# Optimization experiments

Hardware: AMD Instinct MI355X
Metric: run time of the kernel (lower is better)

Reference implementation:

```python
import jax, jax.numpy as jnp
import numpy as np

# EKV constants from Config
VT = 0.025
N_FACTOR = 1.5
VD = 0.5
ALPHA = 2e-06
BASE_TIA = 500000.0

KERNEL = 3
STRIDE = 1
PAD = 1


def _unfold(x, k, stride, pad):
    # torch.nn.functional.unfold: (N, C, H, W) -> (N, C*k*k, L), patch dims ordered (c, kh, kw)
    N, C, H, W = x.shape
    xp = jnp.pad(x, ((0, 0), (0, 0), (pad, pad), (pad, pad)))
    Ho = (H + 2 * pad - k) // stride + 1
    Wo = (W + 2 * pad - k) // stride + 1
    patches = []
    for i in range(k):
        for j in range(k):
            patches.append(xp[:, :, i:i + stride * Ho:stride, j:j + stride * Wo:stride])
    # (k*k, N, C, Ho, Wo) -> (N, C, k*k, Ho*Wo) -> (N, C*k*k, L)
    p = jnp.stack(patches, axis=2)  # (N, C, k*k, Ho, Wo)
    return p.reshape(N, C * k * k, Ho * Wo), Ho, Wo


def setup_inputs() -> dict:
    key = jax.random.key(0)
    k1, k2 = jax.random.split(key)
    x = jax.random.normal(k1, (4, 64, 32, 32), dtype=jnp.float32)
    # theta ~ Normal(2.5, 0.5), shape (out_channels, in_channels, k, k)
    theta = 2.5 + 0.5 * jax.random.normal(k2, (64, 64, 3, 3), dtype=jnp.float32)
    return {"x": x, "theta": theta}


def reference(x, theta):
    N, C, H, W = x.shape
    O = theta.shape[0]
    fan_in = C * KERNEL * KERNEL
    tia_gain = BASE_TIA / (fan_in ** 0.5)
    phi = 2 * N_FACTOR * VT

    x_unf, Ho, Wo = _unfold(x, KERNEL, STRIDE, PAD)      # (N, C*k*k, L)
    x_in = x_unf[:, None, :, :]                           # (N, 1, CKK, L)
    w_th = theta.reshape(1, O, -1, 1)                     # (1, O, CKK, 1)

    v_diff = x_in - w_th                                  # (N, O, CKK, L)
    f_term = jnp.square(jax.nn.softplus(v_diff / phi))
    r_term = jnp.square(jax.nn.softplus((v_diff - VD) / phi))
    i_syn = ALPHA * (f_term - r_term)
    out_current = jnp.sum(i_syn, axis=2)                  # (N, O, L)
    out_voltage = out_current * tia_gain
    return out_voltage.reshape(N, O, Ho, Wo)
```

## Files before the change

### kernel.cpp

```cpp
#include <hip/hip_runtime.h>
#include <math.h>

#define HH 32
#define WW 32
#define CIN 64
#define NO 64
#define NCK 576
#define X_ELEMS 262144
#define STRIDE_E 296

#define WS_W    0
#define WS_TAU  36864

__device__ __forceinline__ float fexp2(float x) {
#if __has_builtin(__builtin_amdgcn_exp2f)
    return __builtin_amdgcn_exp2f(x);
#else
    return exp2f(x);
#endif
}
__device__ __forceinline__ float flog2(float x) {
#if __has_builtin(__builtin_amdgcn_logf)
    return __builtin_amdgcn_logf(x);
#else
    return log2f(x);
#endif
}

__global__ __launch_bounds__(256) void prep_kernel(const float* __restrict__ theta,
                                                   float* __restrict__ ws) {
    constexpr float SZ = 19.235933878519512f;
    const int b = blockIdx.x, t = threadIdx.x;
    if (b < 144) {
        int i = b * 256 + t;
        int o = i & 63, ck = i >> 6;
        float th = theta[o * NCK + ck];
        ws[WS_W + i] = -SZ * th;
        float mn = th;
#pragma unroll
        for (int s = 32; s > 0; s >>= 1)
            mn = fminf(mn, __shfl_xor(mn, s, 64));
        if (o == 0) ws[WS_TAU + ck] = SZ * mn - 8.0f;
    } else {
        if (t < 64) ws[WS_TAU + NCK + t] = 1e30f;
    }
}

__global__ __launch_bounds__(512) void ekv_kernel(
        const float* __restrict__ x, const float* __restrict__ ws,
        float* __restrict__ out) {
    constexpr float SZ = 19.235933878519512f;
    constexpr float C2 = 1.2726342e-3f;
    constexpr float OS = 0.020018875579925058f;

    __shared__ int   lc[8][STRIDE_E];
    __shared__ float lx[8][STRIDE_E];
    __shared__ float pp[8][64];

    const int t    = threadIdx.x;
    const int lane = t & 63;
    const int wv   = __builtin_amdgcn_readfirstlane(t >> 6);
    const int p2   = (int)blockIdx.x * 8 + wv;
    const int pix  = p2 >> 1, half = p2 & 1;
    const int n  = pix >> 10;
    const int ho = (pix >> 5) & 31;
    const int wo = pix & 31;
    const int c0 = half * 32;

    int l = lane;
    int c_off = l / 9; if (c_off > 6) c_off = 6;
    int k = l - 9 * c_off; if (k > 8) k = 8;
    int di = k / 3, dj = k - 3 * (k / 3);
    int h = ho + di - 1, w_ = wo + dj - 1;
    bool sval = (h >= 0) && (h < HH) && (w_ >= 0) && (w_ < WW);
    int hc = min(max(h, 0), HH - 1), wc = min(max(w_, 0), WW - 1);
    float msc = ((l < 63) && sval) ? SZ : 0.0f;

    int gidx = n * (CIN * HH * WW) + (c0 + c_off) * 1024 + hc * WW + wc;
    const float* tw = ws + WS_TAU + c0 * 9;

    int cnt = 0;
    float xv = x[min(gidx, X_ELEMS - 1)];
    float tv = tw[l];

    for (int cb = 0; cb < 32; cb += 7) {
        int cc = 32 - cb; if (cc > 7) cc = 7;
        int gidx2 = gidx + 7 * 1024;
        const float* tw2 = tw + 63;
        float xvn = xv, tvn = tv;
        if (cb + 7 < 32) { xvn = x[min(gidx2, X_ELEMS - 1)]; tvn = tw2[l]; }

        float xs = xv * msc;
        bool a = (xs >= tv) && (l < cc * 9);
        unsigned long long act = __ballot(a);
        unsigned lo32 = (unsigned)act, hi32 = (unsigned)(act >> 32);
        int idx = __builtin_amdgcn_mbcnt_hi(hi32,
                      __builtin_amdgcn_mbcnt_lo(lo32, 0));
        if (a) {
            lc[wv][cnt + idx] = (c0 + cb) * 9 + l;
            lx[wv][cnt + idx] = xs;
        }
        cnt += (int)__popcll(act);
        gidx = gidx2; tw = tw2; xv = xvn; tv = tvn;
    }
    int padn = (-cnt) & 7;
    if (lane < padn) { lc[wv][cnt + lane] = 0; lx[wv][cnt + lane] = -100000.0f; }
    const int rounds = (cnt + padn) >> 3;

    const int4*   LC = (const int4*)&lc[wv][0];
    const float4* LX = (const float4*)&lx[wv][0];
    const float* wsW = ws + WS_W + lane;

    float accF0 = 0.f, accR0 = 0.f, accF1 = 0.f, accR1 = 0.f;

#define EKV_BODY(SX, WV, AF, AR)                                           \
    {                                                                      \
        float z  = (WV) + (SX);                        \
        float e  = fexp2(z);                                               \
        float f  = flog2(1.0f + e);                                        \
        float rr = flog2(fmaf(C2, e, 1.0f));                               \
        AF = fmaf(f, f, AF);                                               \
        AR = fmaf(rr, rr, AR);                                             \
    }

    if (rounds > 0) {
        int4   ca = LC[0], cb4 = LC[1];
        float4 xa = LX[0], xb = LX[1];
        for (int r = 0; r < rounds; ++r) {
            int4 can = ca, cbn = cb4; float4 xan = xa, xbn = xb;
            if (r + 1 < rounds) {
                can = LC[2 * r + 2]; cbn = LC[2 * r + 3];
                xan = LX[2 * r + 2]; xbn = LX[2 * r + 3];
            }
            float W0 = wsW[ca.x  << 6];
            float W1 = wsW[ca.y  << 6];
            float W2 = wsW[ca.z  << 6];
            float W3 = wsW[ca.w  << 6];
            float W4 = wsW[cb4.x << 6];
            float W5 = wsW[cb4.y << 6];
            float W6 = wsW[cb4.z << 6];
            float W7 = wsW[cb4.w << 6];
            EKV_BODY(xa.x, W0, accF0, accR0)
            EKV_BODY(xa.y, W1, accF1, accR1)
            EKV_BODY(xa.z, W2, accF0, accR0)
            EKV_BODY(xa.w, W3, accF1, accR1)
            EKV_BODY(xb.x, W4, accF0, accR0)
            EKV_BODY(xb.y, W5, accF1, accR1)
            EKV_BODY(xb.z, W6, accF0, accR0)
            EKV_BODY(xb.w, W7, accF1, accR1)
            ca = can; cb4 = cbn; xa = xan; xb = xbn;
        }
    }
#undef EKV_BODY

    pp[wv][lane] = (accF0 + accF1) - (accR0 + accR1);
    __syncthreads();
    if (t < 64) {
        float s0 = (pp[0][t] + pp[1][t]) * OS;
        float s1 = (pp[2][t] + pp[3][t]) * OS;
        float s2 = (pp[4][t] + pp[5][t]) * OS;
        float s3 = (pp[6][t] + pp[7][t]) * OS;
        int pixb = (int)blockIdx.x * 4;
        int nn = pixb >> 10, hh = (pixb >> 5) & 31, w0 = pixb & 31;
        float4 v = make_float4(s0, s1, s2, s3);
        *(float4*)&out[((nn * NO + t) * HH + hh) * WW + w0] = v;
    }
}

extern "C" void kernel_launch(void* const* d_in, const int* in_sizes, int n_in,
                              void* d_out, int out_size, void* d_ws, size_t ws_size,
                              hipStream_t stream) {
    const float* x     = (const float*)d_in[0];
    const float* theta = (const float*)d_in[1];
    float* out = (float*)d_out;
    float* ws  = (float*)d_ws;

    prep_kernel<<<145, 256, 0, stream>>>(theta, ws);
    ekv_kernel <<<1024, 512, 0, stream>>>(x, ws, out);
}
```

Measured before the change: 73.21 us.

## Fuse prep and EKV kernels into one cooperative launch with grid sync

Merges the theta-preprocessing kernel and the main EKV kernel into a single cooperative kernel. The first 73 blocks write the scaled weights and thresholds, then a grid-wide sync makes them visible before compute. The grid is halved to 512 blocks, and each block now handles two pixel units of 8 waves and writes two float4 outputs. This removes one kernel launch and the gap between the two kernels. In exchange it adds a grid barrier, needs all 512 blocks to be co-resident, and gives each block more serial work.

```diff
diff --git a/kernel.cpp b/kernel.cpp
--- a/kernel.cpp
+++ b/kernel.cpp
@@ -1,5 +1,8 @@
 #include <hip/hip_runtime.h>
+#include <hip/hip_cooperative_groups.h>
 #include <math.h>
+
+namespace cg = cooperative_groups;
 
 #define HH 32
 #define WW 32
@@ -27,12 +30,24 @@
 #endif
 }
 
-__global__ __launch_bounds__(256) void prep_kernel(const float* __restrict__ theta,
-                                                   float* __restrict__ ws) {
+__global__ __launch_bounds__(512, 4) void ekv_fused(
+        const float* __restrict__ x, const float* __restrict__ theta,
+        float* __restrict__ ws, float* __restrict__ out) {
     constexpr float SZ = 19.235933878519512f;
-    const int b = blockIdx.x, t = threadIdx.x;
-    if (b < 144) {
-        int i = b * 256 + t;
+    constexpr float C2 = 1.2726342e-3f;
+    constexpr float OS = 0.020018875579925058f;
+
+    __shared__ int   lc[8][STRIDE_E];
+    __shared__ float lx[8][STRIDE_E];
+    __shared__ float pp[16][64];
+
+    const int t    = threadIdx.x;
+    const int lane = t & 63;
+    const int wv   = __builtin_amdgcn_readfirstlane(t >> 6);
+    const int bb   = (int)blockIdx.x;
+
+    if (bb < 72) {
+        int i = bb * 512 + t;
         int o = i & 63, ck = i >> 6;
         float th = theta[o * NCK + ck];
         ws[WS_W + i] = -SZ * th;
@@ -41,129 +56,124 @@
         for (int s = 32; s > 0; s >>= 1)
             mn = fminf(mn, __shfl_xor(mn, s, 64));
         if (o == 0) ws[WS_TAU + ck] = SZ * mn - 8.0f;
-    } else {
+    } else if (bb == 72) {
         if (t < 64) ws[WS_TAU + NCK + t] = 1e30f;
     }
-}
+    __threadfence();
+    cg::this_grid().sync();
 
-__global__ __launch_bounds__(512) void ekv_kernel(
-        const float* __restrict__ x, const float* __restrict__ ws,
-        float* __restrict__ out) {
-    constexpr float SZ = 19.235933878519512f;
-    constexpr float C2 = 1.2726342e-3f;
-    constexpr float OS = 0.020018875579925058f;
+    for (int unit = 0; unit < 2; ++unit) {
+        const int p2  = bb * 16 + wv + unit * 8;
+        const int pix = p2 >> 1, half = p2 & 1;
+        const int n  = pix >> 10;
+        const int ho = (pix >> 5) & 31;
+        const int wo = pix & 31;
+        const int c0 = half * 32;
 
-    __shared__ int   lc[8][STRIDE_E];
-    __shared__ float lx[8][STRIDE_E];
-    __shared__ float pp[8][64];
+        int l = lane;
+        int c_off = l / 9; if (c_off > 6) c_off = 6;
+        int k = l - 9 * c_off; if (k > 8) k = 8;
+        int di = k / 3, dj = k - 3 * (k / 3);
+        int h = ho + di - 1, w_ = wo + dj - 1;
+        bool sval = (h >= 0) && (h < HH) && (w_ >= 0) && (w_ < WW);
+        int hc = min(max(h, 0), HH - 1), wc = min(max(w_, 0), WW - 1);
+        float msc = ((l < 63) && sval) ? SZ : 0.0f;
 
-    const int t    = threadIdx.x;
-    const int lane = t & 63;
-    const int wv   = __builtin_amdgcn_readfirstlane(t >> 6);
-    const int p2   = (int)blockIdx.x * 8 + wv;
-    const int pix  = p2 >> 1, half = p2 & 1;
-    const int n  = pix >> 10;
-    const int ho = (pix >> 5) & 31;
-    const int wo = pix & 31;
-    const int c0 = half * 32;
+        int gidx = n * (CIN * HH * WW) + (c0 + c_off) * 1024 + hc * WW + wc;
+        const float* tw = ws + WS_TAU + c0 * 9;
 
-    int l = lane;
-    int c_off = l / 9; if (c_off > 6) c_off = 6;
-    int k = l - 9 * c_off; if (k > 8) k = 8;
-    int di = k / 3, dj = k - 3 * (k / 3);
-    int h = ho + di - 1, w_ = wo + dj - 1;
-    bool sval = (h >= 0) && (h < HH) && (w_ >= 0) && (w_ < WW);
-    int hc = min(max(h, 0), HH - 1), wc = min(max(w_, 0), WW - 1);
-    float msc = ((l < 63) && sval) ? SZ : 0.0f;
+        int cnt = 0;
+        float xv = x[min(gidx, X_ELEMS - 1)];
+        float tv = tw[l];
 
-    int gidx = n * (CIN * HH * WW) + (c0 + c_off) * 1024 + hc * WW + wc;
-    const float* tw = ws + WS_TAU + c0 * 9;
+        for (int cb = 0; cb < 32; cb += 7) {
+            int cc = 32 - cb; if (cc > 7) cc = 7;
+            int gidx2 = gidx + 7 * 1024;
+            const float* tw2 = tw + 63;
+            float xvn = xv, tvn = tv;
+            if (cb + 7 < 32) { xvn = x[min(gidx2, X_ELEMS - 1)]; tvn = tw2[l]; }
 
-    int cnt = 0;
-    float xv = x[min(gidx, X_ELEMS - 1)];
-    float tv = tw[l];
+            float xs = xv * msc;
+            bool a = (xs >= tv) && (l < cc * 9);
+            unsigned long long act = __ballot(a);
+            unsigned lo32 = (unsigned)act, hi32 = (unsigned)(act >> 32);
+            int idx = __builtin_amdgcn_mbcnt_hi(hi32,
+                          __builtin_amdgcn_mbcnt_lo(lo32, 0));
+            if (a) {
+                lc[wv][cnt + idx] = (c0 + cb) * 9 + l;
+                lx[wv][cnt + idx] = xs;
+            }
+            cnt += (int)__popcll(act);
+            gidx = gidx2; tw = tw2; xv = xvn; tv = tvn;
+        }
+        int padn = (-cnt) & 7;
+        if (lane < padn) { lc[wv][cnt + lane] = 0; lx[wv][cnt + lane] = -100000.0f; }
+        const int rounds = (cnt + padn) >> 3;
 
-    for (int cb = 0; cb < 32; cb += 7) {
-        int cc = 32 - cb; if (cc > 7) cc = 7;
-        int gidx2 = gidx + 7 * 1024;
-        const float* tw2 = tw + 63;
-        float xvn = xv, tvn = tv;
-        if (cb + 7 < 32) { xvn = x[min(gidx2, X_ELEMS - 1)]; tvn = tw2[l]; }
+        const int4*   LC = (const int4*)&lc[wv][0];
+        const float4* LX = (const float4*)&lx[wv][0];
+        const float* wsW = ws + WS_W + lane;
 
-        float xs = xv * msc;
-        bool a = (xs >= tv) && (l < cc * 9);
-        unsigned long long act = __ballot(a);
-        unsigned lo32 = (unsigned)act, hi32 = (unsigned)(act >> 32);
-        int idx = __builtin_amdgcn_mbcnt_hi(hi32,
-                      __builtin_amdgcn_mbcnt_lo(lo32, 0));
-        if (a) {
-            lc[wv][cnt + idx] = (c0 + cb) * 9 + l;
-            lx[wv][cnt + idx] = xs;
-        }
-        cnt += (int)__popcll(act);
-        gidx = gidx2; tw = tw2; xv = xvn; tv = tvn;
-    }
-    int padn = (-cnt) & 7;
-    if (lane < padn) { lc[wv][cnt + lane] = 0; lx[wv][cnt + lane] = -100000.0f; }
-    const int rounds = (cnt + padn) >> 3;
-
-    const int4*   LC = (const int4*)&lc[wv][0];
-    const float4* LX = (const float4*)&lx[wv][0];
-    const float* wsW = ws + WS_W + lane;
-
-    float accF0 = 0.f, accR0 = 0.f, accF1 = 0.f, accR1 = 0.f;
+        float accF0 = 0.f, accR0 = 0.f, accF1 = 0.f, accR1 = 0.f;
 
 #define EKV_BODY(SX, WV, AF, AR)                                           \
-    {                                                                      \
-        float z  = (WV) + (SX);                        \
-        float e  = fexp2(z);                                               \
-        float f  = flog2(1.0f + e);                                        \
-        float rr = flog2(fmaf(C2, e, 1.0f));                               \
-        AF = fmaf(f, f, AF);                                               \
-        AR = fmaf(rr, rr, AR);                                             \
+        {                                                                  \
+            float z  = (WV) + (SX);                    \
+            float e  = fexp2(z);                                           \
+            float f  = flog2(1.0f + e);                                    \
+            float rr = flog2(fmaf(C2, e, 1.0f));                           \
+            AF = fmaf(f, f, AF);                                           \
+            AR = fmaf(rr, rr, AR);                                         \
+        }
+
+        if (rounds > 0) {
+            int4   ca = LC[0], cb4 = LC[1];
+            float4 xa = LX[0], xb = LX[1];
+            for (int r = 0; r < rounds; ++r) {
+                int4 can = ca, cbn = cb4; float4 xan = xa, xbn = xb;
+                if (r + 1 < rounds) {
+                    can = LC[2 * r + 2]; cbn = LC[2 * r + 3];
+                    xan = LX[2 * r + 2]; xbn = LX[2 * r + 3];
+                }
+                float W0 = wsW[ca.x  << 6];
+                float W1 = wsW[ca.y  << 6];
+                float W2 = wsW[ca.z  << 6];
+                float W3 = wsW[ca.w  << 6];
+                float W4 = wsW[cb4.x << 6];
+                float W5 = wsW[cb4.y << 6];
+                float W6 = wsW[cb4.z << 6];
+                float W7 = wsW[cb4.w << 6];
+                EKV_BODY(xa.x, W0, accF0, accR0)
+                EKV_BODY(xa.y, W1, accF1, accR1)
+                EKV_BODY(xa.z, W2, accF0, accR0)
+                EKV_BODY(xa.w, W3, accF1, accR1)
+                EKV_BODY(xb.x, W4, accF0, accR0)
+                EKV_BODY(xb.y, W5, accF1, accR1)
+                EKV_BODY(xb.z, W6, accF0, accR0)
+                EKV_BODY(xb.w, W7, accF1, accR1)
+                ca = can; cb4 = cbn; xa = xan; xb = xbn;
+            }
+        }
+#undef EKV_BODY
+
+        pp[wv + unit * 8][lane] = (accF0 + accF1) - (accR0 + accR1);
     }
 
-    if (rounds > 0) {
-        int4   ca = LC[0], cb4 = LC[1];
-        float4 xa = LX[0], xb = LX[1];
-        for (int r = 0; r < rounds; ++r) {
-            int4 can = ca, cbn = cb4; float4 xan = xa, xbn = xb;
-            if (r + 1 < rounds) {
-                can = LC[2 * r + 2]; cbn = LC[2 * r + 3];
-                xan = LX[2 * r + 2]; xbn = LX[2 * r + 3];
-            }
-            float W0 = wsW[ca.x  << 6];
-            float W1 = wsW[ca.y  << 6];
-            float W2 = wsW[ca.z  << 6];
-            float W3 = wsW[ca.w  << 6];
-            float W4 = wsW[cb4.x << 6];
-            float W5 = wsW[cb4.y << 6];
-            float W6 = wsW[cb4.z << 6];
-            float W7 = wsW[cb4.w << 6];
-            EKV_BODY(xa.x, W0, accF0, accR0)
-            EKV_BODY(xa.y, W1, accF1, accR1)
-            EKV_BODY(xa.z, W2, accF0, accR0)
-            EKV_BODY(xa.w, W3, accF1, accR1)
-            EKV_BODY(xb.x, W4, accF0, accR0)
-            EKV_BODY(xb.y, W5, accF1, accR1)
-            EKV_BODY(xb.z, W6, accF0, accR0)
-            EKV_BODY(xb.w, W7, accF1, accR1)
-            ca = can; cb4 = cbn; xa = xan; xb = xbn;
-        }
-    }
-#undef EKV_BODY
-
-    pp[wv][lane] = (accF0 + accF1) - (accR0 + accR1);
     __syncthreads();
     if (t < 64) {
-        float s0 = (pp[0][t] + pp[1][t]) * OS;
-        float s1 = (pp[2][t] + pp[3][t]) * OS;
-        float s2 = (pp[4][t] + pp[5][t]) * OS;
-        float s3 = (pp[6][t] + pp[7][t]) * OS;
-        int pixb = (int)blockIdx.x * 4;
+        float s0 = (pp[ 0][t] + pp[ 1][t]) * OS;
+        float s1 = (pp[ 2][t] + pp[ 3][t]) * OS;
+        float s2 = (pp[ 4][t] + pp[ 5][t]) * OS;
+        float s3 = (pp[ 6][t] + pp[ 7][t]) * OS;
+        float s4 = (pp[ 8][t] + pp[ 9][t]) * OS;
+        float s5 = (pp[10][t] + pp[11][t]) * OS;
+        float s6 = (pp[12][t] + pp[13][t]) * OS;
+        float s7 = (pp[14][t] + pp[15][t]) * OS;
+        int pixb = bb * 8;
         int nn = pixb >> 10, hh = (pixb >> 5) & 31, w0 = pixb & 31;
-        float4 v = make_float4(s0, s1, s2, s3);
-        *(float4*)&out[((nn * NO + t) * HH + hh) * WW + w0] = v;
+        float* po = &out[((nn * NO + t) * HH + hh) * WW + w0];
+        *(float4*)(po)     = make_float4(s0, s1, s2, s3);
+        *(float4*)(po + 4) = make_float4(s4, s5, s6, s7);
     }
 }
 
@@ -175,6 +185,7 @@
     float* out = (float*)d_out;
     float* ws  = (float*)d_ws;
 
-    prep_kernel<<<145, 256, 0, stream>>>(theta, ws);
-    ekv_kernel <<<1024, 512, 0, stream>>>(x, ws, out);
+    void* args[] = { (void*)&x, (void*)&theta, (void*)&ws, (void*)&out };
+    hipLaunchCooperativeKernel((const void*)ekv_fused, dim3(512), dim3(512),
+                               args, 0, stream);
 }
```

Result: slower. 173.6 us (+137.2%).
